# Optimization experiments

Measured on AMD Instinct MI355X. Metric: run time of the kernel, lower is better.

Reference implementation:

```python
import jax, jax.numpy as jnp
import numpy as np

BN_EPS = 1e-5


def setup_inputs() -> dict:
    key = jax.random.key(0)
    ks = jax.random.split(key, 8)
    B, C, H, W = 8, 256, 64, 64
    Cqk = C // 8  # query/key channels = out_channels // 8
    x = jax.random.normal(ks[0], (B, C, H, W), dtype=jnp.float32)
    # 1x1 convs == per-pixel matmuls; kaiming-normal-ish scale
    wq = jax.random.normal(ks[1], (Cqk, C), dtype=jnp.float32) * np.sqrt(2.0 / C)
    bq = jnp.zeros((Cqk,), dtype=jnp.float32)
    wk = jax.random.normal(ks[2], (Cqk, C), dtype=jnp.float32) * np.sqrt(2.0 / C)
    bk = jnp.zeros((Cqk,), dtype=jnp.float32)
    wv = jax.random.normal(ks[3], (C, C), dtype=jnp.float32) * np.sqrt(2.0 / C)
    bv = jnp.zeros((C,), dtype=jnp.float32)
    # gamma is initialized to 0 in the original; use a small nonzero value so
    # the attention path actually contributes (and has nontrivial gradients)
    gamma = jnp.full((1,), 0.5, dtype=jnp.float32)
    bn_weight = jnp.ones((C,), dtype=jnp.float32)
    bn_bias = jnp.zeros((C,), dtype=jnp.float32)
    return {"x": x, "wq": wq, "bq": bq, "wk": wk, "bk": bk,
            "wv": wv, "bv": bv, "gamma": gamma,
            "bn_weight": bn_weight, "bn_bias": bn_bias}


def reference(x, wq, bq, wk, bk, wv, bv, gamma, bn_weight, bn_bias):
    B, C, H, W = x.shape
    N = H * W
    xf = x.reshape(B, C, N)  # (B, C, N)
    # 1x1 conv projections as channel matmuls
    q = jnp.einsum('oc,bcn->bno', wq, xf) + bq            # (B, N, Cqk)
    k = jnp.einsum('oc,bcn->bon', wk, xf) + bk[:, None]   # (B, Cqk, N)
    v = jnp.einsum('oc,bcn->bon', wv, xf) + bv[:, None]   # (B, C, N)
    # attention[b, i, j] = softmax_j(q_i . k_j)  -- full N x N matrix
    scores = jnp.einsum('bno,bom->bnm', q, k)             # (B, N, N)
    attn = jax.nn.softmax(scores, axis=2)
    # out[b, c, i] = sum_j v[b, c, j] * attn[b, i, j]
    out = jnp.einsum('bcj,bij->bci', v, attn)             # (B, C, N)
    out = out.reshape(B, C, H, W)
    out = gamma[0] * out + x
    # BatchNorm2d in training mode: batch statistics over (B, H, W)
    mean = jnp.mean(out, axis=(0, 2, 3), keepdims=True)
    var = jnp.var(out, axis=(0, 2, 3), keepdims=True)
    out = (out - mean) * jax.lax.rsqrt(var + BN_EPS)
    out = out * bn_weight[None, :, None, None] + bn_bias[None, :, None, None]
    return jax.nn.relu(out)
```

## Files before the change

kernel.cpp:

```cpp
#include <hip/hip_runtime.h>
#include <stdint.h>

#define B_ 8
#define C_ 256
#define N_ 4096
#define CQK 32
#define VPANEL (C_ * 64)
#define BPSTRIDE 520

#define PSTRIDE 272
#define PBUF    17408
#define KSTRIDE 40
#define KBUF    5120

typedef __attribute__((ext_vector_type(8))) _Float16 f16x8;
typedef __attribute__((ext_vector_type(4))) float f32x4;

__device__ __forceinline__ unsigned short f2bf_rne(float f) {
  unsigned u = __builtin_bit_cast(unsigned, f);
  u += 0x7FFFu + ((u >> 16) & 1u);
  return (unsigned short)(u >> 16);
}

__device__ __forceinline__ float fexp2(float x) {
  float r; asm("v_exp_f32 %0, %1" : "=v"(r) : "v"(x)); return r;
}

__global__ __launch_bounds__(256) void wconv_kernel(
    const float* __restrict__ wq, const float* __restrict__ wk,
    const float* __restrict__ wv, _Float16* __restrict__ wf,
    float* __restrict__ stats)
{
  int idx = blockIdx.x * 256 + threadIdx.x;
  if (idx < 4096) stats[idx] = 0.f;
  int e = idx * 4;
  int o = e >> 8, c = e & 255;
  const float* src;
  if (o < 32)      src = wq + o * 256 + c;
  else if (o < 64) src = wk + (o - 32) * 256 + c;
  else             src = wv + (o - 64) * 256 + c;
  float4 v = *(const float4*)src;
  _Float16 h[4] = {(_Float16)v.x, (_Float16)v.y, (_Float16)v.z, (_Float16)v.w};
  *(uint2*)(wf + e) = *(uint2*)h;
}

__global__ __launch_bounds__(256, 2) void proj_fused_kernel(
    const float* __restrict__ x, const _Float16* __restrict__ wf,
    const float* __restrict__ bq, const float* __restrict__ bk,
    const float* __restrict__ bv,
    _Float16* __restrict__ qf, _Float16* __restrict__ kf,
    _Float16* __restrict__ vout)
{
  __shared__ float xs[2][64 * 65];
  __shared__ _Float16 bp[32 * BPSTRIDE];

  const int t = threadIdx.x, lane = t & 63;
  const int w = t >> 6;
  const int l15 = lane & 15, q4 = lane >> 4;
  const int blk = blockIdx.x;
  const int b  = blk & 7;
  const int nt = blk >> 3;
  const int n0 = nt * 64;
  const int o0w = (w & 1) * 32;
  const int n0w = (w >> 1) * 32;

  const int cc = (t >> 4);
  const int nn = (t & 15) * 4;

  {
    float4 v0[4];
    #pragma unroll
    for (int p = 0; p < 4; ++p)
      v0[p] = *(const float4*)(x + ((size_t)(b * C_) + p * 16 + cc) * N_ + n0 + nn);
    #pragma unroll
    for (int p = 0; p < 4; ++p) {
      float* dst = &xs[0][(p * 16 + cc) * 65 + nn];
      dst[0] = v0[p].x; dst[1] = v0[p].y; dst[2] = v0[p].z; dst[3] = v0[p].w;
    }
  }
  __syncthreads();

  for (int ct = 0; ct < 4; ++ct) {
    float4 vn[4];
    if (ct < 3) {
      #pragma unroll
      for (int p = 0; p < 4; ++p)
        vn[p] = *(const float4*)(x + ((size_t)(b * C_) + (ct + 1) * 64 + p * 16 + cc) * N_ + n0 + nn);
    }
    #pragma unroll
    for (int h = 0; h < 2; ++h) {
      int oct = w + h * 4;
      int n = lane;
      _Float16 hh[8];
      #pragma unroll
      for (int j = 0; j < 8; ++j) hh[j] = (_Float16)xs[ct & 1][(oct * 8 + j) * 65 + n];
      *(f16x8*)(bp + (size_t)(ct * 8 + oct) * BPSTRIDE + n * 8) = *(f16x8*)hh;
    }
    if (ct < 3) {
      #pragma unroll
      for (int p = 0; p < 4; ++p) {
        float* dst = &xs[(ct + 1) & 1][(p * 16 + cc) * 65 + nn];
        dst[0] = vn[p].x; dst[1] = vn[p].y; dst[2] = vn[p].z; dst[3] = vn[p].w;
      }
      __syncthreads();
    }
  }
  __syncthreads();

  const f32x4 zf = {0.f, 0.f, 0.f, 0.f};
  for (int otile = 0; otile < 5; ++otile) {
    f32x4 acc[2][2];
    #pragma unroll
    for (int a = 0; a < 2; ++a)
      #pragma unroll
      for (int bb = 0; bb < 2; ++bb) acc[a][bb] = zf;

    const _Float16* wbase = wf + (size_t)(otile * 64 + o0w) * 256;

    #pragma unroll 2
    for (int kc = 0; kc < 8; ++kc) {
      f16x8 af[2], bfr[2];
      #pragma unroll
      for (int ob = 0; ob < 2; ++ob)
        af[ob] = *(const f16x8*)(wbase + (ob * 16 + l15) * 256 + kc * 32 + q4 * 8);
      #pragma unroll
      for (int nb = 0; nb < 2; ++nb)
        bfr[nb] = *(const f16x8*)(bp + (size_t)(kc * 4 + q4) * BPSTRIDE + (n0w + nb * 16 + l15) * 8);
      #pragma unroll
      for (int ob = 0; ob < 2; ++ob)
        #pragma unroll
        for (int nb = 0; nb < 2; ++nb)
          acc[ob][nb] = __builtin_amdgcn_mfma_f32_16x16x32_f16(af[ob], bfr[nb], acc[ob][nb], 0, 0, 0);
    }

    if (otile == 0) {
      _Float16* dst = (o0w == 0) ? qf : kf;
      const float* bias = (o0w == 0) ? bq : bk;
      const float qsc = (o0w == 0) ? 1.4426950408889634f : 1.0f;
      #pragma unroll
      for (int ob = 0; ob < 2; ++ob) {
        float4 b4 = *(const float4*)(bias + ob * 16 + q4 * 4);
        #pragma unroll
        for (int nb = 0; nb < 2; ++nb) {
          int pixel = n0 + n0w + nb * 16 + l15;
          _Float16 h[4];
          h[0] = (_Float16)((acc[ob][nb][0] + b4.x) * qsc);
          h[1] = (_Float16)((acc[ob][nb][1] + b4.y) * qsc);
          h[2] = (_Float16)((acc[ob][nb][2] + b4.z) * qsc);
          h[3] = (_Float16)((acc[ob][nb][3] + b4.w) * qsc);
          *(uint2*)(dst + ((size_t)(b * N_) + pixel) * CQK + ob * 16 + q4 * 4) = *(uint2*)h;
        }
      }
    } else {
      int cbase = (otile - 1) * 64 + o0w;
      _Float16* vpan = vout + ((size_t)(b * 64 + nt)) * VPANEL;
      #pragma unroll
      for (int ob = 0; ob < 2; ++ob) {
        float4 b4 = *(const float4*)(bv + cbase + ob * 16 + q4 * 4);
        #pragma unroll
        for (int nb = 0; nb < 2; ++nb) {
          int jj = n0w + nb * 16 + l15;
          #pragma unroll
          for (int r = 0; r < 4; ++r) {
            int c = cbase + ob * 16 + q4 * 4 + r;
            float bval = (r == 0) ? b4.x : (r == 1) ? b4.y : (r == 2) ? b4.z : b4.w;
            vpan[(size_t)c * 64 + jj] = (_Float16)(acc[ob][nb][r] + bval);
          }
        }
      }
    }
  }
}

#define ATTN_BODY(K, BUF) do { \
   \
  f16x8 ks_[2]; \
  { const _Float16* kg_ = kstage + (size_t)(((K) + 1) & 31) * (128 * CQK); \
    _Pragma("unroll") \
    for (int s = 0; s < 2; ++s) { \
      int idx_ = s * 256 + t; \
      ks_[s] = *(const f16x8*)(kg_ + (idx_ >> 2) * CQK + (idx_ & 3) * 8); } } \
   \
  f16x8 vx_[16]; \
  { const _Float16* vp_ = vbase + (size_t)(K) * 2 * VPANEL; \
    _Pragma("unroll") \
    for (int ks = 0; ks < 4; ++ks) \
      _Pragma("unroll") \
      for (int cb = 0; cb < 4; ++cb) \
        vx_[ks * 4 + cb] = *(const f16x8*)(vp_ + (ks >> 1) * VPANEL + cb * 1024 + (ks & 1) * 32); } \
   \
  f16x8 kx_[8]; \
  { const _Float16* kl_ = Klds + ((K) & 1) * KBUF + l15 * KSTRIDE + q4 * 8; \
    _Pragma("unroll") \
    for (int jb = 0; jb < 8; ++jb) kx_[jb] = *(const f16x8*)(kl_ + jb * (16 * KSTRIDE)); } \
  f32x4 sv_[8]; \
  _Pragma("unroll") \
  for (int jb = 0; jb < 8; ++jb) \
    sv_[jb] = __builtin_amdgcn_mfma_f32_16x16x32_f16(kx_[jb], qfr, zf, 0, 0, 0); \
  float pm_[8]; \
  _Pragma("unroll") \
  for (int jb = 0; jb < 8; ++jb) \
    pm_[jb] = fmaxf(fmaxf(sv_[jb][0], sv_[jb][1]), fmaxf(sv_[jb][2], sv_[jb][3])); \
  float ra_ = fmaxf(fmaxf(pm_[0], pm_[1]), pm_[2]); \
  float rb_ = fmaxf(fmaxf(pm_[3], pm_[4]), pm_[5]); \
  float rc_ = fmaxf(fmaxf(pm_[6], pm_[7]), ra_); \
  float lm_ = fmaxf(rb_, rc_); \
  lm_ = fmaxf(lm_, __shfl_xor(lm_, 16)); \
  lm_ = fmaxf(lm_, __shfl_xor(lm_, 32)); \
  bool upd_ = lm_ > mold + 8.0f; \
  unsigned long long bal_ = __ballot(upd_);      \
  float alpha_ = upd_ ? fexp2(mold - lm_) : 1.0f; \
  if (upd_) mold = lm_; \
  float ts_ = 0.f; \
  { char* pb_ = (char*)Plds + (BUF) * PBUF + (w * 16 + l15) * PSTRIDE + q4 * 8; \
    _Pragma("unroll") \
    for (int jb = 0; jb < 8; ++jb) { \
      float p0_ = fexp2(sv_[jb][0] - mold), p1_ = fexp2(sv_[jb][1] - mold); \
      float p2_ = fexp2(sv_[jb][2] - mold), p3_ = fexp2(sv_[jb][3] - mold); \
      ts_ += (p0_ + p1_) + (p2_ + p3_); \
      _Float16 h_[4] = {(_Float16)p0_, (_Float16)p1_, (_Float16)p2_, (_Float16)p3_}; \
      *(uint2*)(pb_ + jb * 32) = *(uint2*)h_; } } \
   \
  { _Float16* kw_ = Klds + (((K) + 1) & 1) * KBUF; \
    _Pragma("unroll") \
    for (int s = 0; s < 2; ++s) { \
      int idx_ = s * 256 + t; \
      *(f16x8*)(kw_ + (idx_ >> 2) * KSTRIDE + (idx_ & 3) * 8) = ks_[s]; } } \
  if (q4 == 0) alphal[(BUF) * 64 + w * 16 + l15] = alpha_; \
  if (lane == 0) flagw[(BUF) * 4 + w] = (bal_ != 0ull) ? 1 : 0; \
  ts_ += __shfl_xor(ts_, 16); \
  ts_ += __shfl_xor(ts_, 32); \
  lrun = lrun * alpha_ + ts_; \
  asm volatile("s_waitcnt lgkmcnt(0)" ::: "memory"); \
  __builtin_amdgcn_sched_barrier(0); \
  __builtin_amdgcn_s_barrier(); \
  asm volatile("" ::: "memory"); \
  { int4 fl_ = *(const int4*)(flagw + (BUF) * 4); \
    if (fl_.x | fl_.y | fl_.z | fl_.w) { \
      _Pragma("unroll") \
      for (int ib = 0; ib < 4; ++ib) { \
        float av_ = alphal[(BUF) * 64 + ib * 16 + l15]; \
        _Pragma("unroll") \
        for (int cb = 0; cb < 4; ++cb) \
          _Pragma("unroll") \
          for (int r = 0; r < 4; ++r) acc[cb][ib][r] *= av_; } } } \
  __builtin_amdgcn_s_setprio(1); \
  _Pragma("unroll") \
  for (int ks = 0; ks < 4; ++ks) { \
    f16x8 pf_[4]; \
    _Pragma("unroll") \
    for (int ib = 0; ib < 4; ++ib) \
      pf_[ib] = *(const f16x8*)((char*)Plds + (BUF) * PBUF + (ib * 16 + l15) * PSTRIDE + ks * 64 + q4 * 16); \
    _Pragma("unroll") \
    for (int cb = 0; cb < 4; ++cb) \
      _Pragma("unroll") \
      for (int ib = 0; ib < 4; ++ib) \
        acc[cb][ib] = __builtin_amdgcn_mfma_f32_16x16x32_f16(vx_[ks * 4 + cb], pf_[ib], acc[cb][ib], 0, 0, 0); \
  } \
  __builtin_amdgcn_s_setprio(0); \
} while (0)

__global__ __launch_bounds__(256, 2) void attn_kernel(
    const float* __restrict__ x, const float* __restrict__ gptr,
    const _Float16* __restrict__ qf, const _Float16* __restrict__ kf,
    const _Float16* __restrict__ vf, unsigned short* __restrict__ yout,
    float* __restrict__ stats)
{
  __shared__ __align__(16) char smem[56096];
  _Float16* Plds  = (_Float16*)smem;
  _Float16* Klds  = (_Float16*)(smem + 34816);
  float* alphal = (float*)(smem + 55296);
  int*   flagw  = (int*)(smem + 55808);
  float* lrowl  = (float*)(smem + 55840);

  const int t = threadIdx.x, lane = t & 63;
  const int w = t >> 6;
  const int l15 = lane & 15, q4 = lane >> 4;
  const int b  = blockIdx.x & 7;
  const int it = blockIdx.x >> 3;
  const int i0 = it * 64;
  const float gamma = gptr[0];

  const f16x8 qfr = *(const f16x8*)(qf + ((size_t)(b * N_) + i0 + w * 16 + l15) * CQK + q4 * 8);

  const _Float16* kstage = kf + (size_t)b * N_ * CQK;
  const _Float16* vbase = vf + (size_t)b * (64 * VPANEL)
                             + ((size_t)(w * 64 + l15)) * 64 + q4 * 8;

  f32x4 acc[4][4];
  const f32x4 zf = {0.f, 0.f, 0.f, 0.f};
  #pragma unroll
  for (int a = 0; a < 4; ++a)
    #pragma unroll
    for (int bb = 0; bb < 4; ++bb) acc[a][bb] = zf;

  float mold = -1e30f, lrun = 0.f;

  #pragma unroll
  for (int s = 0; s < 2; ++s) {
    int idx = s * 256 + t;
    f16x8 v = *(const f16x8*)(kstage + (idx >> 2) * CQK + (idx & 3) * 8);
    *(f16x8*)(Klds + (idx >> 2) * KSTRIDE + (idx & 3) * 8) = v;
  }
  __syncthreads();

  #pragma unroll 1
  for (int k = 0; k < 32; k += 2) {
    ATTN_BODY(k, 0);
    ATTN_BODY(k + 1, 1);
  }

  if (q4 == 0) lrowl[w * 16 + l15] = lrun;
  __syncthreads();
  float linv[4];
  #pragma unroll
  for (int ib = 0; ib < 4; ++ib) linv[ib] = 1.0f / lrowl[ib * 16 + l15];

  float* sb = stats + b * 512;
  #pragma unroll
  for (int cb = 0; cb < 4; ++cb) {
    #pragma unroll
    for (int r = 0; r < 4; ++r) {
      int c = w * 64 + cb * 16 + q4 * 4 + r;
      float s1 = 0.f, s2 = 0.f;
      #pragma unroll
      for (int ib = 0; ib < 4; ++ib) {
        int i = i0 + ib * 16 + l15;
        size_t off = ((size_t)(b * C_) + c) * N_ + i;
        float y = fmaf(gamma, acc[cb][ib][r] * linv[ib], x[off]);
        yout[off] = f2bf_rne(y);
        s1 += y;
        s2 += y * y;
      }
      #pragma unroll
      for (int m = 1; m < 16; m <<= 1) {
        s1 += __shfl_xor(s1, m);
        s2 += __shfl_xor(s2, m);
      }
      if (l15 == 0) {
        atomicAdd(sb + c, s1);
        atomicAdd(sb + 256 + c, s2);
      }
    }
  }
}

__global__ __launch_bounds__(256) void bnapply_kernel(
    const unsigned short* __restrict__ y, float* __restrict__ out,
    const float* __restrict__ stats,
    const float* __restrict__ bnw, const float* __restrict__ bnb)
{
  size_t idx = (size_t)blockIdx.x * 256 + threadIdx.x;
  size_t el = idx * 8;
  int c = (int)((el >> 12) & 255);
  float s1 = 0.f, s2 = 0.f;
  #pragma unroll
  for (int bb = 0; bb < 8; ++bb) {
    s1 += stats[bb * 512 + c];
    s2 += stats[bb * 512 + 256 + c];
  }
  float mean = s1 * (1.0f / 32768.0f);
  float var  = fmaf(-mean, mean, s2 * (1.0f / 32768.0f));
  float rstd = rsqrtf(var + 1e-5f);
  float sc = bnw[c] * rstd;
  float sh = fmaf(-mean, sc, bnb[c]);
  uint4 u = *(const uint4*)(y + el);
  unsigned uu[4] = {u.x, u.y, u.z, u.w};
  float4 o0, o1;
  float v[8];
  #pragma unroll
  for (int k = 0; k < 4; ++k) {
    v[2 * k]     = __builtin_bit_cast(float, uu[k] << 16);
    v[2 * k + 1] = __builtin_bit_cast(float, uu[k] & 0xFFFF0000u);
  }
  o0.x = fmaxf(fmaf(v[0], sc, sh), 0.f);
  o0.y = fmaxf(fmaf(v[1], sc, sh), 0.f);
  o0.z = fmaxf(fmaf(v[2], sc, sh), 0.f);
  o0.w = fmaxf(fmaf(v[3], sc, sh), 0.f);
  o1.x = fmaxf(fmaf(v[4], sc, sh), 0.f);
  o1.y = fmaxf(fmaf(v[5], sc, sh), 0.f);
  o1.z = fmaxf(fmaf(v[6], sc, sh), 0.f);
  o1.w = fmaxf(fmaf(v[7], sc, sh), 0.f);
  *(float4*)(out + el) = o0;
  *(float4*)(out + el + 4) = o1;
}

extern "C" void kernel_launch(void* const* d_in, const int* in_sizes, int n_in,
                              void* d_out, int out_size, void* d_ws, size_t ws_size,
                              hipStream_t stream)
{
  const float* x   = (const float*)d_in[0];
  const float* wq  = (const float*)d_in[1];
  const float* bq  = (const float*)d_in[2];
  const float* wk  = (const float*)d_in[3];
  const float* bk  = (const float*)d_in[4];
  const float* wv  = (const float*)d_in[5];
  const float* bv  = (const float*)d_in[6];
  const float* gm  = (const float*)d_in[7];
  const float* bnw = (const float*)d_in[8];
  const float* bnb = (const float*)d_in[9];
  float* out = (float*)d_out;

  _Float16* vfp = (_Float16*)((char*)d_out + (size_t)B_ * C_ * N_ * 2);

  char* ws = (char*)d_ws;
  _Float16* qf = (_Float16*)(ws);
  _Float16* kf = (_Float16*)(ws + ((size_t)2 << 20));
  unsigned short* yout = (unsigned short*)(ws + ((size_t)4 << 20));
  _Float16* wf = (_Float16*)(ws + ((size_t)21 << 20));
  float* stats = (float*)(ws + ((size_t)22 << 20));

  hipLaunchKernelGGL(wconv_kernel, dim3(80), dim3(256), 0, stream,
                     wq, wk, wv, wf, stats);
  hipLaunchKernelGGL(proj_fused_kernel, dim3(512), dim3(256), 0, stream,
                     x, wf, bq, bk, bv, qf, kf, vfp);
  hipLaunchKernelGGL(attn_kernel, dim3(512), dim3(256), 0, stream,
                     x, gm, qf, kf, vfp, yout, stats);
  hipLaunchKernelGGL(bnapply_kernel, dim3(4096), dim3(256), 0, stream,
                     yout, out, stats, bnw, bnb);
}
```

Before: 259.9 us.

## Halve projection pixel tile to 32 to double block count and occupancy

The fused QKV projection kernel now handles 32 pixels per block instead of 64, launching 1024 blocks with a smaller LDS footprint and a launch bound of 4 blocks per CU. Each wave now computes a 16-output-row by 32-pixel slice, and the V panel writes are remapped to half-panels. The aim is better latency hiding and more parallelism in the projection stage, which previously ran only 512 blocks. In exchange, weight reads are spread over more blocks and each block does less MFMA work per weight load.

```diff
diff --git a/kernel.cpp b/kernel.cpp
--- a/kernel.cpp
+++ b/kernel.cpp
@@ -6,7 +6,9 @@
 #define N_ 4096
 #define CQK 32
 #define VPANEL (C_ * 64)
-#define BPSTRIDE 520
+
+#define XSTRIDE 33
+#define BP2STRIDE 264
 
 #define PSTRIDE 272
 #define PBUF    17408
@@ -44,15 +46,15 @@
   *(uint2*)(wf + e) = *(uint2*)h;
 }
 
-__global__ __launch_bounds__(256, 2) void proj_fused_kernel(
+__global__ __launch_bounds__(256, 4) void proj_fused_kernel(
     const float* __restrict__ x, const _Float16* __restrict__ wf,
     const float* __restrict__ bq, const float* __restrict__ bk,
     const float* __restrict__ bv,
     _Float16* __restrict__ qf, _Float16* __restrict__ kf,
     _Float16* __restrict__ vout)
 {
-  __shared__ float xs[2][64 * 65];
-  __shared__ _Float16 bp[32 * BPSTRIDE];
+  __shared__ float xs[2][64 * XSTRIDE];
+  __shared__ _Float16 bp[32 * BP2STRIDE];
 
   const int t = threadIdx.x, lane = t & 63;
   const int w = t >> 6;
@@ -60,48 +62,38 @@
   const int blk = blockIdx.x;
   const int b  = blk & 7;
   const int nt = blk >> 3;
-  const int n0 = nt * 64;
-  const int o0w = (w & 1) * 32;
-  const int n0w = (w >> 1) * 32;
-
-  const int cc = (t >> 4);
-  const int nn = (t & 15) * 4;
+  const int n0 = nt * 32;
+
+  const int cc = t >> 2;
+  const int nn = (t & 3) * 8;
+  const int oct = t >> 5;
+  const int tn  = t & 31;
 
   {
-    float4 v0[4];
-    #pragma unroll
-    for (int p = 0; p < 4; ++p)
-      v0[p] = *(const float4*)(x + ((size_t)(b * C_) + p * 16 + cc) * N_ + n0 + nn);
-    #pragma unroll
-    for (int p = 0; p < 4; ++p) {
-      float* dst = &xs[0][(p * 16 + cc) * 65 + nn];
-      dst[0] = v0[p].x; dst[1] = v0[p].y; dst[2] = v0[p].z; dst[3] = v0[p].w;
-    }
+    float4 v0 = *(const float4*)(x + ((size_t)(b * C_) + cc) * N_ + n0 + nn);
+    float4 v1 = *(const float4*)(x + ((size_t)(b * C_) + cc) * N_ + n0 + nn + 4);
+    float* dst = &xs[0][cc * XSTRIDE + nn];
+    dst[0] = v0.x; dst[1] = v0.y; dst[2] = v0.z; dst[3] = v0.w;
+    dst[4] = v1.x; dst[5] = v1.y; dst[6] = v1.z; dst[7] = v1.w;
   }
   __syncthreads();
 
   for (int ct = 0; ct < 4; ++ct) {
-    float4 vn[4];
+    float4 va, vb2;
     if (ct < 3) {
-      #pragma unroll
-      for (int p = 0; p < 4; ++p)
-        vn[p] = *(const float4*)(x + ((size_t)(b * C_) + (ct + 1) * 64 + p * 16 + cc) * N_ + n0 + nn);
-    }
-    #pragma unroll
-    for (int h = 0; h < 2; ++h) {
-      int oct = w + h * 4;
-      int n = lane;
+      va  = *(const float4*)(x + ((size_t)(b * C_) + (ct + 1) * 64 + cc) * N_ + n0 + nn);
+      vb2 = *(const float4*)(x + ((size_t)(b * C_) + (ct + 1) * 64 + cc) * N_ + n0 + nn + 4);
+    }
+    {
       _Float16 hh[8];
       #pragma unroll
-      for (int j = 0; j < 8; ++j) hh[j] = (_Float16)xs[ct & 1][(oct * 8 + j) * 65 + n];
-      *(f16x8*)(bp + (size_t)(ct * 8 + oct) * BPSTRIDE + n * 8) = *(f16x8*)hh;
+      for (int j = 0; j < 8; ++j) hh[j] = (_Float16)xs[ct & 1][(oct * 8 + j) * XSTRIDE + tn];
+      *(f16x8*)(bp + (size_t)(ct * 8 + oct) * BP2STRIDE + tn * 8) = *(f16x8*)hh;
     }
     if (ct < 3) {
-      #pragma unroll
-      for (int p = 0; p < 4; ++p) {
-        float* dst = &xs[(ct + 1) & 1][(p * 16 + cc) * 65 + nn];
-        dst[0] = vn[p].x; dst[1] = vn[p].y; dst[2] = vn[p].z; dst[3] = vn[p].w;
-      }
+      float* dst = &xs[(ct + 1) & 1][cc * XSTRIDE + nn];
+      dst[0] = va.x; dst[1] = va.y; dst[2] = va.z; dst[3] = va.w;
+      dst[4] = vb2.x; dst[5] = vb2.y; dst[6] = vb2.z; dst[7] = vb2.w;
       __syncthreads();
     }
   }
@@ -109,63 +101,50 @@
 
   const f32x4 zf = {0.f, 0.f, 0.f, 0.f};
   for (int otile = 0; otile < 5; ++otile) {
-    f32x4 acc[2][2];
-    #pragma unroll
-    for (int a = 0; a < 2; ++a)
-      #pragma unroll
-      for (int bb = 0; bb < 2; ++bb) acc[a][bb] = zf;
-
-    const _Float16* wbase = wf + (size_t)(otile * 64 + o0w) * 256;
+    f32x4 acc2[2];
+    acc2[0] = zf; acc2[1] = zf;
+
+    const _Float16* wbase = wf + (size_t)(otile * 64 + w * 16) * 256;
 
     #pragma unroll 2
     for (int kc = 0; kc < 8; ++kc) {
-      f16x8 af[2], bfr[2];
-      #pragma unroll
-      for (int ob = 0; ob < 2; ++ob)
-        af[ob] = *(const f16x8*)(wbase + (ob * 16 + l15) * 256 + kc * 32 + q4 * 8);
+      f16x8 af = *(const f16x8*)(wbase + l15 * 256 + kc * 32 + q4 * 8);
+      f16x8 bfr[2];
       #pragma unroll
       for (int nb = 0; nb < 2; ++nb)
-        bfr[nb] = *(const f16x8*)(bp + (size_t)(kc * 4 + q4) * BPSTRIDE + (n0w + nb * 16 + l15) * 8);
-      #pragma unroll
-      for (int ob = 0; ob < 2; ++ob)
-        #pragma unroll
-        for (int nb = 0; nb < 2; ++nb)
-          acc[ob][nb] = __builtin_amdgcn_mfma_f32_16x16x32_f16(af[ob], bfr[nb], acc[ob][nb], 0, 0, 0);
+        bfr[nb] = *(const f16x8*)(bp + (size_t)(kc * 4 + q4) * BP2STRIDE + (nb * 16 + l15) * 8);
+      #pragma unroll
+      for (int nb = 0; nb < 2; ++nb)
+        acc2[nb] = __builtin_amdgcn_mfma_f32_16x16x32_f16(af, bfr[nb], acc2[nb], 0, 0, 0);
     }
 
     if (otile == 0) {
-      _Float16* dst = (o0w == 0) ? qf : kf;
-      const float* bias = (o0w == 0) ? bq : bk;
-      const float qsc = (o0w == 0) ? 1.4426950408889634f : 1.0f;
-      #pragma unroll
-      for (int ob = 0; ob < 2; ++ob) {
-        float4 b4 = *(const float4*)(bias + ob * 16 + q4 * 4);
-        #pragma unroll
-        for (int nb = 0; nb < 2; ++nb) {
-          int pixel = n0 + n0w + nb * 16 + l15;
-          _Float16 h[4];
-          h[0] = (_Float16)((acc[ob][nb][0] + b4.x) * qsc);
-          h[1] = (_Float16)((acc[ob][nb][1] + b4.y) * qsc);
-          h[2] = (_Float16)((acc[ob][nb][2] + b4.z) * qsc);
-          h[3] = (_Float16)((acc[ob][nb][3] + b4.w) * qsc);
-          *(uint2*)(dst + ((size_t)(b * N_) + pixel) * CQK + ob * 16 + q4 * 4) = *(uint2*)h;
-        }
+      _Float16* dst = (w < 2) ? qf : kf;
+      const float* bias = (w < 2) ? bq : bk;
+      const float qsc = (w < 2) ? 1.4426950408889634f : 1.0f;
+      float4 b4 = *(const float4*)(bias + (w & 1) * 16 + q4 * 4);
+      #pragma unroll
+      for (int nb = 0; nb < 2; ++nb) {
+        int pixel = n0 + nb * 16 + l15;
+        _Float16 h[4];
+        h[0] = (_Float16)((acc2[nb][0] + b4.x) * qsc);
+        h[1] = (_Float16)((acc2[nb][1] + b4.y) * qsc);
+        h[2] = (_Float16)((acc2[nb][2] + b4.z) * qsc);
+        h[3] = (_Float16)((acc2[nb][3] + b4.w) * qsc);
+        *(uint2*)(dst + ((size_t)(b * N_) + pixel) * CQK + (w & 1) * 16 + q4 * 4) = *(uint2*)h;
       }
     } else {
-      int cbase = (otile - 1) * 64 + o0w;
-      _Float16* vpan = vout + ((size_t)(b * 64 + nt)) * VPANEL;
-      #pragma unroll
-      for (int ob = 0; ob < 2; ++ob) {
-        float4 b4 = *(const float4*)(bv + cbase + ob * 16 + q4 * 4);
+      int cbase = (otile - 1) * 64 + w * 16;
+      _Float16* vpan = vout + ((size_t)(b * 64 + (nt >> 1))) * VPANEL;
+      float4 b4 = *(const float4*)(bv + cbase + q4 * 4);
+      #pragma unroll
+      for (int nb = 0; nb < 2; ++nb) {
+        int jj = (nt & 1) * 32 + nb * 16 + l15;
         #pragma unroll
-        for (int nb = 0; nb < 2; ++nb) {
-          int jj = n0w + nb * 16 + l15;
-          #pragma unroll
-          for (int r = 0; r < 4; ++r) {
-            int c = cbase + ob * 16 + q4 * 4 + r;
-            float bval = (r == 0) ? b4.x : (r == 1) ? b4.y : (r == 2) ? b4.z : b4.w;
-            vpan[(size_t)c * 64 + jj] = (_Float16)(acc[ob][nb][r] + bval);
-          }
+        for (int r = 0; r < 4; ++r) {
+          int c = cbase + q4 * 4 + r;
+          float bval = (r == 0) ? b4.x : (r == 1) ? b4.y : (r == 2) ? b4.z : b4.w;
+          vpan[(size_t)c * 64 + jj] = (_Float16)(acc2[nb][r] + bval);
         }
       }
     }
@@ -412,7 +391,7 @@
 
   hipLaunchKernelGGL(wconv_kernel, dim3(80), dim3(256), 0, stream,
                      wq, wk, wv, wf, stats);
-  hipLaunchKernelGGL(proj_fused_kernel, dim3(512), dim3(256), 0, stream,
+  hipLaunchKernelGGL(proj_fused_kernel, dim3(1024), dim3(256), 0, stream,
                      x, wf, bq, bk, bv, qf, kf, vfp);
   hipLaunchKernelGGL(attn_kernel, dim3(512), dim3(256), 0, stream,
                      x, gm, qf, kf, vfp, yout, stats);
```

After: 263.1 us. Within noise of the previous version (+1.2%).
